# Kernel optimization log

Measured on AMD Instinct MI355X. Metric: run time of the kernel, lower is better.

## Reference

```python
import jax, jax.numpy as jnp
import numpy as np

HEADS = 8
DIM_HEAD = 64
RADIUS = 0.2
NSAMPLE = 8
EPS = 1e-5


def setup_inputs() -> dict:
    key = jax.random.key(0)
    ks = jax.random.split(key, 6)
    b, l, n, dim = 2, 4, 1024, 512
    inner = HEADS * DIM_HEAD
    xyzs = jax.random.uniform(ks[0], (b, l, n, 3), jnp.float32)
    feature = jax.random.normal(ks[1], (b, l, n, dim), jnp.float32)
    gamma = jnp.ones((dim,), jnp.float32)
    beta = jnp.zeros((dim,), jnp.float32)
    w_qkv = jax.random.normal(ks[2], (dim, 3 * inner), jnp.float32) * 0.02
    w_spatial = jax.random.normal(ks[3], (3, DIM_HEAD), jnp.float32) * 0.02
    w_out = jax.random.normal(ks[4], (inner, dim), jnp.float32) * 0.02
    b_out = jnp.zeros((dim,), jnp.float32)
    return {"xyzs": xyzs, "feature": feature, "gamma": gamma, "beta": beta,
            "w_qkv": w_qkv, "w_spatial": w_spatial, "w_out": w_out, "b_out": b_out}


def ball_query(ref, query):
    """pointnet2-style ball query. ref:(B,N,3), query:(B,M,3) -> (B,M,NSAMPLE) int32.
    Takes the first (lowest-index) NSAMPLE in-radius points, pads with the first
    found index; all-zeros if no point is in radius (matches CUDA kernel)."""
    d2 = jnp.sum((query[:, :, None, :] - ref[:, None, :, :]) ** 2, axis=-1)  # (B,M,N)
    mask = d2 < RADIUS ** 2
    nref = ref.shape[1]
    score = jnp.where(mask, -jnp.arange(nref, dtype=jnp.float32), -jnp.inf)
    vals, pos = jax.lax.top_k(score, NSAMPLE)  # smallest in-radius indices first
    valid = vals > -jnp.inf
    first = jnp.where(valid[..., :1], pos[..., :1], 0)
    return jnp.where(valid, pos, first)


def _forward(xyzs, feature, gamma, beta, w_qkv, w_spatial, w_out, b_out):
    b, l, n, dim = feature.shape
    h, dh = HEADS, DIM_HEAD
    inner = h * dh
    scale = dh ** -0.5
    # LayerNorm over channel dim
    mu = jnp.mean(feature, -1, keepdims=True)
    var = jnp.var(feature, -1, keepdims=True)
    normf = (feature - mu) * jax.lax.rsqrt(var + EPS) * gamma + beta
    qkv = normf @ w_qkv
    q, k, v = jnp.split(qkv, 3, axis=-1)          # each (b, l, n, inner)
    xyz_flat = xyzs.reshape(b * l, n, 3)
    k_flat = k.reshape(b * l, n, inner)
    v_flat = v.reshape(b * l, n, inner)
    bidx = jnp.arange(b * l)[:, None, None]

    def per_frame(q_i, xyz_i):
        # q_i: (b, n, inner) queries of frame i; xyz_i: (b, n, 3)
        # frame-i points query neighbors inside every frame of the video
        qxyz = jnp.broadcast_to(xyz_i[:, None], (b, l, n, 3)).reshape(b * l, n, 3)
        idx = ball_query(xyz_flat, qxyz)           # (b*l, n, 8)
        g_k = k_flat[bidx, idx]                    # (b*l, n, 8, inner)
        g_v = v_flat[bidx, idx]
        g_xyz = xyz_flat[bidx, idx]                # (b*l, n, 8, 3)
        disp = g_xyz - qxyz[:, :, None]            # (b*l, n, 8, 3)
        # '(b l) n k (h d) -> b n h (l k) d'
        keys = g_k.reshape(b, l, n, NSAMPLE, h, dh).transpose(0, 2, 4, 1, 3, 5).reshape(b, n, h, l * NSAMPLE, dh)
        vals = g_v.reshape(b, l, n, NSAMPLE, h, dh).transpose(0, 2, 4, 1, 3, 5).reshape(b, n, h, l * NSAMPLE, dh)
        qh = q_i.reshape(b, n, h, dh)
        logits = jnp.einsum('bnhd,bnhjd->bnhj', qh, keys) * scale
        attn = jax.nn.softmax(logits, axis=-1)     # (b, n, h, l*8)
        # 'b l n k d -> b n (l k) d'
        dis = disp.reshape(b, l, n, NSAMPLE, 3).transpose(0, 2, 1, 3, 4).reshape(b, n, l * NSAMPLE, 3)
        dis_attn = jnp.max(attn[..., None] * dis[:, :, None], axis=3)  # (b, n, h, 3)
        dis_attn = (dis_attn @ w_spatial).reshape(b, n, inner)         # spatial_op
        attnout = jnp.einsum('bnhj,bnhjd->bnhd', attn, vals).reshape(b, n, inner)
        return attnout + dis_attn

    q_frames = jnp.moveaxis(q, 1, 0)               # (l, b, n, inner)
    xyz_frames = jnp.moveaxis(xyzs, 1, 0)          # (l, b, n, 3)
    frames = jax.vmap(per_frame)(q_frames, xyz_frames)   # (l, b, n, inner)
    frame_result = jnp.moveaxis(frames, 0, 1)      # (b, l, n, inner)
    out = jax.nn.gelu(frame_result @ w_out + b_out, approximate=False)
    return out + feature


def reference(xyzs, feature, gamma, beta, w_qkv, w_spatial, w_out, b_out):
    return _forward(xyzs, feature, gamma, beta, w_qkv, w_spatial, w_out, b_out)
```

## Files before the change

### kernel.cpp

```cpp
#include <hip/hip_runtime.h>
#include <hip/hip_bf16.h>

#define B_ 2
#define L_ 4
#define N_ 1024
#define DIM_ 512
#define INNER_ 512
#define HEADS_ 8
#define DH_ 64
#define NS_ 8
#define NFR_ (B_ * L_)
#define ROWS_ (B_ * L_ * N_)

typedef unsigned short u16;
typedef __attribute__((ext_vector_type(8))) short bf16x8;
typedef __attribute__((ext_vector_type(4))) float f32x4;

__device__ inline float bf2f(u16 u) {
    union { unsigned i; float f; } c; c.i = ((unsigned)u) << 16; return c.f;
}
__device__ inline float bflo(unsigned v) {
    union { unsigned i; float f; } c; c.i = v << 16; return c.f;
}
__device__ inline float bfhi(unsigned v) {
    union { unsigned i; float f; } c; c.i = v & 0xffff0000u; return c.f;
}
__device__ inline u16 f2bf(float x) {
    __hip_bfloat16 h = __float2bfloat16(x);
    return *reinterpret_cast<u16*>(&h);
}

#if __has_builtin(__builtin_amdgcn_fdot2_f32_bf16)
typedef __bf16 bf2v __attribute__((ext_vector_type(2)));
__device__ inline float dot8(bf16x8 a, bf16x8 b, float acc) {
    union U { bf16x8 v; bf2v p[4]; };
    U ua, ub; ua.v = a; ub.v = b;
    #pragma unroll
    for (int i = 0; i < 4; ++i)
        acc = __builtin_amdgcn_fdot2_f32_bf16(ua.p[i], ub.p[i], acc, false);
    return acc;
}
#else
__device__ inline float dot8(bf16x8 a, bf16x8 b, float acc) {
    #pragma unroll
    for (int e = 0; e < 8; ++e) acc += bf2f((u16)a[e]) * bf2f((u16)b[e]);
    return acc;
}
#endif

__global__ __launch_bounds__(256) void transpose_cvt(
    const float* __restrict__ wqkv, const float* __restrict__ wout,
    u16* __restrict__ wqkvT, u16* __restrict__ woutT)
{
    const float* src; u16* dst; int R, C, tr, tc;
    int b = blockIdx.x;
    if (b < 192) { src = wqkv; dst = wqkvT; R = 512; C = 1536; tr = b / 24; tc = b % 24; }
    else { b -= 192; src = wout; dst = woutT; R = 512; C = 512; tr = b / 8; tc = b % 8; }
    int r0 = tr * 64, c0 = tc * 64;
    int t = threadIdx.x;

    __shared__ float tile[64][65];

    int rr = t >> 2, cs = (t & 3) * 16;
    const float* sp = src + (size_t)(r0 + rr) * C + c0 + cs;
    #pragma unroll
    for (int e = 0; e < 16; e += 4) {
        f32x4 v = *(const f32x4*)(sp + e);
        tile[rr][cs + e + 0] = v[0];
        tile[rr][cs + e + 1] = v[1];
        tile[rr][cs + e + 2] = v[2];
        tile[rr][cs + e + 3] = v[3];
    }
    __syncthreads();

    int c = t >> 2, ks = (t & 3) * 16;
    u16 outv[16];
    #pragma unroll
    for (int e = 0; e < 16; ++e) outv[e] = f2bf(tile[ks + e][c]);
    u16* dp = dst + (size_t)(c0 + c) * R + r0 + ks;
    *(bf16x8*)(dp)     = *(bf16x8*)&outv[0];
    *(bf16x8*)(dp + 8) = *(bf16x8*)&outv[8];
}

__global__ __launch_bounds__(256) void ln_kernel(
    const float* __restrict__ f, const float* __restrict__ g,
    const float* __restrict__ b, u16* __restrict__ o)
{
    int row = blockIdx.x;
    int t = threadIdx.x;
    const float* fr = f + (size_t)row * DIM_;
    float x0 = fr[t], x1 = fr[t + 256];

    __shared__ float red[4];
    float s = x0 + x1;
    #pragma unroll
    for (int off = 32; off; off >>= 1) s += __shfl_xor(s, off, 64);
    if ((t & 63) == 0) red[t >> 6] = s;
    __syncthreads();
    float mu = (red[0] + red[1] + red[2] + red[3]) * (1.0f / 512.0f);
    __syncthreads();

    float d0 = x0 - mu, d1 = x1 - mu;
    float q = d0 * d0 + d1 * d1;
    #pragma unroll
    for (int off = 32; off; off >>= 1) q += __shfl_xor(q, off, 64);
    if ((t & 63) == 0) red[t >> 6] = q;
    __syncthreads();
    float var = (red[0] + red[1] + red[2] + red[3]) * (1.0f / 512.0f);
    float inv = rsqrtf(var + 1e-5f);

    o[(size_t)row * DIM_ + t]       = f2bf(d0 * inv * g[t]       + b[t]);
    o[(size_t)row * DIM_ + t + 256] = f2bf(d1 * inv * g[t + 256] + b[t + 256]);
}

__global__ __launch_bounds__(256) void gemm_bt(
    const u16* __restrict__ A, const u16* __restrict__ Bt,
    u16* __restrict__ Cb16, float* __restrict__ Cf32,
    int M, int N, int K, int nb128, int mode,
    const float* __restrict__ bias, const float* __restrict__ resid)
{
    __shared__ u16 As[128 * 40];
    __shared__ u16 Bs[128 * 40];

    int bx = blockIdx.x % nb128;
    int by = blockIdx.x / nb128;
    int m0 = by * 128, n0 = bx * 128;
    int t = threadIdx.x;
    int wave = t >> 6, lane = t & 63;
    int lr = lane & 15, quad = lane >> 4;
    int wm = (wave >> 1) * 64, wn = (wave & 1) * 64;

    f32x4 acc[4][4];
    #pragma unroll
    for (int i = 0; i < 4; ++i)
        #pragma unroll
        for (int j = 0; j < 4; ++j)
            acc[i][j] = {0.f, 0.f, 0.f, 0.f};

    for (int k0 = 0; k0 < K; k0 += 32) {
        #pragma unroll
        for (int p = 0; p < 2; ++p) {
            int c = t + p * 256;
            int r = c >> 2;
            int kc = (c & 3) * 8;
            *(bf16x8*)&As[r * 40 + kc] = *(const bf16x8*)(A + (size_t)(m0 + r) * K + k0 + kc);
            *(bf16x8*)&Bs[r * 40 + kc] = *(const bf16x8*)(Bt + (size_t)(n0 + r) * K + k0 + kc);
        }
        __syncthreads();

        bf16x8 af[4], bfr[4];
        #pragma unroll
        for (int mb = 0; mb < 4; ++mb)
            af[mb] = *(const bf16x8*)&As[(wm + mb * 16 + lr) * 40 + quad * 8];
        #pragma unroll
        for (int nb = 0; nb < 4; ++nb)
            bfr[nb] = *(const bf16x8*)&Bs[(wn + nb * 16 + lr) * 40 + quad * 8];
        #pragma unroll
        for (int mb = 0; mb < 4; ++mb)
            #pragma unroll
            for (int nb = 0; nb < 4; ++nb)
                acc[mb][nb] = __builtin_amdgcn_mfma_f32_16x16x32_bf16(
                    af[mb], bfr[nb], acc[mb][nb], 0, 0, 0);
        __syncthreads();
    }

    #pragma unroll
    for (int mb = 0; mb < 4; ++mb) {
        #pragma unroll
        for (int nb = 0; nb < 4; ++nb) {
            int col = n0 + wn + nb * 16 + lr;
            #pragma unroll
            for (int r = 0; r < 4; ++r) {
                int row = m0 + wm + mb * 16 + quad * 4 + r;
                float x = acc[mb][nb][r];
                if (mode == 1) {
                    x += bias[col];
                    float gl = 0.5f * x * (1.0f + erff(x * 0.70710678118654752f));
                    Cf32[(size_t)row * N + col] = gl + resid[(size_t)row * N + col];
                } else {
                    Cb16[(size_t)row * N + col] = f2bf(x);
                }
            }
        }
    }
}

#define RPAD_(r) ((r) + ((r) >> 4))

__global__ __launch_bounds__(256) void ballq_kernel(
    const float* __restrict__ xyz, int* __restrict__ idxt)
{
    #pragma clang fp contract(off)
    int chunk = blockIdx.x & 255;
    int combo = blockIdx.x >> 8;
    int jf = combo & 3;
    int bi = combo >> 2;

    __shared__ float rx[N_ + (N_ >> 4)], ry[N_ + (N_ >> 4)], rz[N_ + (N_ >> 4)];
    const float* ref = xyz + (size_t)((bi * L_ + jf) * N_) * 3;
    for (int p = threadIdx.x; p < N_; p += 256) {
        rx[RPAD_(p)] = ref[p * 3 + 0];
        ry[RPAD_(p)] = ref[p * 3 + 1];
        rz[RPAD_(p)] = ref[p * 3 + 2];
    }
    __syncthreads();

    int wave = threadIdx.x >> 6;
    int lane = threadIdx.x & 63;
    int n = chunk * 4 + wave;
    int base = lane * 17;
    int r0 = lane * 16;

    for (int qi = 0; qi < L_; ++qi) {
        const float* qp = xyz + (size_t)((bi * L_ + qi) * N_ + n) * 3;
        float qx = qp[0], qy = qp[1], qz = qp[2];

        unsigned mask = 0;
        #pragma unroll
        for (int j = 0; j < 16; ++j) {
            float dx = qx - rx[base + j];
            float dy = qy - ry[base + j];
            float dz = qz - rz[base + j];
            float d2 = dx * dx + dy * dy;
            d2 = d2 + dz * dz;
            if (d2 < 0.04f) mask |= (1u << j);
        }

        int cnt = __popc(mask);
        int x = cnt;
        #pragma unroll
        for (int off = 1; off < 64; off <<= 1) {
            int y = __shfl_up(x, off, 64);
            if (lane >= off) x += y;
        }
        int pre = x - cnt;
        int total = __shfl(x, 63, 64);

        int localFirst = mask ? (r0 + __builtin_ctz(mask)) : 0x7fffffff;
        int gfirst = localFirst;
        #pragma unroll
        for (int off = 32; off; off >>= 1) gfirst = min(gfirst, __shfl_xor(gfirst, off, 64));

        int* o = idxt + ((size_t)((qi * B_ + bi) * N_ + n)) * 32 + jf * NS_;

        unsigned m = mask;
        int pos = pre;
        while (m && pos < NS_) {
            int j = __builtin_ctz(m);
            o[pos] = r0 + j;
            m &= m - 1;
            ++pos;
        }
        if (lane == 0) {
            int padv = (total > 0) ? gfirst : 0;
            for (int s = (total < NS_ ? total : NS_); s < NS_; ++s) o[s] = padv;
        }
    }
}

__global__ __launch_bounds__(256, 4) void attn_kernel(
    const float* __restrict__ xyz, const u16* __restrict__ qkv,
    const int* __restrict__ idxt, const float* __restrict__ wsp,
    u16* __restrict__ fres)
{
    int x = blockIdx.x & 7;
    int bi = x >> 2;
    int qi = x & 3;
    int n = blockIdx.x >> 3;

    int wave = threadIdx.x >> 6;
    int lane = threadIdx.x & 63;
    int hh = lane >> 5;
    int j = lane & 31;
    int h = wave * 2 + hh;
    int jf = j >> 3;

    int qrow = (bi * L_ + qi) * N_ + n;
    int qq = (qi * B_ + bi) * N_ + n;

    __shared__ float a_s[HEADS_][32];
    __shared__ int grow_s[32];
    __shared__ float da_s[HEADS_][3];

    int idx = idxt[(size_t)qq * 32 + j];
    int kr = (bi * L_ + jf) * N_ + idx;

    const u16* qp = qkv + (size_t)qrow * 1536 + h * 64;
    const u16* kp = qkv + (size_t)kr * 1536 + 512 + h * 64;
    bf16x8 qv[8], kv[8];
    #pragma unroll
    for (int c = 0; c < 8; ++c) {
        kv[c] = *(const bf16x8*)(kp + c * 8);
        qv[c] = *(const bf16x8*)(qp + c * 8);
    }
    float nx = xyz[(size_t)kr * 3 + 0];
    float ny = xyz[(size_t)kr * 3 + 1];
    float nz = xyz[(size_t)kr * 3 + 2];
    __builtin_amdgcn_sched_barrier(0);

    float acc = 0.f;
    #pragma unroll
    for (int c = 0; c < 8; ++c) acc = dot8(kv[c], qv[c], acc);
    float lg = acc * 0.125f;

    float mx = lg;
    #pragma unroll
    for (int off = 16; off; off >>= 1) mx = fmaxf(mx, __shfl_xor(mx, off, 64));
    float e = expf(lg - mx);
    float sum = e;
    #pragma unroll
    for (int off = 16; off; off >>= 1) sum += __shfl_xor(sum, off, 64);
    float a = e / sum;
    a_s[h][j] = a;
    if (wave == 0 && hh == 0) grow_s[j] = kr;

    float qx = xyz[(size_t)qrow * 3 + 0];
    float qy = xyz[(size_t)qrow * 3 + 1];
    float qz = xyz[(size_t)qrow * 3 + 2];
    float tx = a * (nx - qx);
    float ty = a * (ny - qy);
    float tz = a * (nz - qz);
    #pragma unroll
    for (int off = 16; off; off >>= 1) {
        tx = fmaxf(tx, __shfl_xor(tx, off, 64));
        ty = fmaxf(ty, __shfl_xor(ty, off, 64));
        tz = fmaxf(tz, __shfl_xor(tz, off, 64));
    }
    if (j == 0) { da_s[h][0] = tx; da_s[h][1] = ty; da_s[h][2] = tz; }

    __syncthreads();

    int dd = (lane & 31) * 2;
    const u16* vbase = qkv + 1024 + h * 64 + dd;
    int rows[32];
    #pragma unroll
    for (int t = 0; t < 32; ++t) rows[t] = grow_s[t];
    unsigned vv[32];
    #pragma unroll
    for (int t = 0; t < 32; ++t)
        vv[t] = *(const unsigned*)(vbase + (size_t)rows[t] * 1536);
    __builtin_amdgcn_sched_barrier(0);

    float o0 = 0.f, o1 = 0.f;
    #pragma unroll
    for (int t = 0; t < 32; ++t) {
        float at = a_s[h][t];
        o0 += at * bflo(vv[t]);
        o1 += at * bfhi(vv[t]);
    }
    float dax = da_s[h][0], day = da_s[h][1], daz = da_s[h][2];
    float sp0 = dax * wsp[dd]     + day * wsp[64 + dd]     + daz * wsp[128 + dd];
    float sp1 = dax * wsp[dd + 1] + day * wsp[64 + dd + 1] + daz * wsp[128 + dd + 1];

    u16* op = fres + (size_t)qrow * INNER_ + h * 64 + dd;
    unsigned outw = (unsigned)f2bf(o0 + sp0) | ((unsigned)f2bf(o1 + sp1) << 16);
    *(unsigned*)op = outw;
}

extern "C" void kernel_launch(void* const* d_in, const int* in_sizes, int n_in,
                              void* d_out, int out_size, void* d_ws, size_t ws_size,
                              hipStream_t stream) {
    const float* xyz   = (const float*)d_in[0];
    const float* feat  = (const float*)d_in[1];
    const float* gamma = (const float*)d_in[2];
    const float* beta  = (const float*)d_in[3];
    const float* wqkv  = (const float*)d_in[4];
    const float* wsp   = (const float*)d_in[5];
    const float* wout  = (const float*)d_in[6];
    const float* bout  = (const float*)d_in[7];
    float* out = (float*)d_out;

    char* ws = (char*)d_ws;
    u16* normf = (u16*)ws;                 ws += (size_t)ROWS_ * DIM_ * 2;
    u16* wqkvT = (u16*)ws;                 ws += (size_t)3 * INNER_ * DIM_ * 2;
    u16* woutT = (u16*)ws;                 ws += (size_t)DIM_ * INNER_ * 2;
    u16* qkv   = (u16*)ws;                 ws += (size_t)ROWS_ * 3 * INNER_ * 2;
    int* idxt  = (int*)ws;                 ws += (size_t)L_ * NFR_ * N_ * NS_ * 4;
    u16* fres  = normf;

    transpose_cvt<<<256, 256, 0, stream>>>(wqkv, wout, wqkvT, woutT);
    ln_kernel<<<ROWS_, 256, 0, stream>>>(feat, gamma, beta, normf);
    gemm_bt<<<64 * 12, 256, 0, stream>>>(normf, wqkvT, qkv, nullptr,
                                         ROWS_, 3 * INNER_, DIM_, 12, 0, nullptr, nullptr);
    ballq_kernel<<<8 * 256, 256, 0, stream>>>(xyz, idxt);
    attn_kernel<<<ROWS_, 256, 0, stream>>>(xyz, qkv, idxt, wsp, fres);
    gemm_bt<<<64 * 4, 256, 0, stream>>>(fres, woutT, nullptr, out,
                                        ROWS_, DIM_, INNER_, 4, 1, bout, feat);
}
```

Measured before the change: 220.9 us.

## Restructure attention kernel to one wave per head with 512 threads

The attention kernel now runs 512 threads per query, one wave per head. QK dot products are split into 8 pieces of 8 channels each, reduced with lane shuffles. The value accumulation gives each lane one output channel instead of two, and neighbor row indices are staged once in shared memory. The aim is more parallelism and fewer registers per thread, at the cost of an extra barrier, narrower 16-bit value loads and more shuffle reductions.

```diff
diff --git a/kernel.cpp b/kernel.cpp
--- a/kernel.cpp
+++ b/kernel.cpp
@@ -18,12 +18,6 @@
 
 __device__ inline float bf2f(u16 u) {
     union { unsigned i; float f; } c; c.i = ((unsigned)u) << 16; return c.f;
-}
-__device__ inline float bflo(unsigned v) {
-    union { unsigned i; float f; } c; c.i = v << 16; return c.f;
-}
-__device__ inline float bfhi(unsigned v) {
-    union { unsigned i; float f; } c; c.i = v & 0xffff0000u; return c.f;
 }
 __device__ inline u16 f2bf(float x) {
     __hip_bfloat16 h = __float2bfloat16(x);
@@ -258,7 +252,7 @@
     }
 }
 
-__global__ __launch_bounds__(256, 4) void attn_kernel(
+__global__ __launch_bounds__(512, 4) void attn_kernel(
     const float* __restrict__ xyz, const u16* __restrict__ qkv,
     const int* __restrict__ idxt, const float* __restrict__ wsp,
     u16* __restrict__ fres)
@@ -268,93 +262,98 @@
     int qi = x & 3;
     int n = blockIdx.x >> 3;
 
-    int wave = threadIdx.x >> 6;
-    int lane = threadIdx.x & 63;
-    int hh = lane >> 5;
-    int j = lane & 31;
-    int h = wave * 2 + hh;
-    int jf = j >> 3;
+    int t = threadIdx.x;
+    int h = t >> 6;
+    int lane = t & 63;
+    int piece = lane >> 3;
+    int jg = lane & 7;
 
     int qrow = (bi * L_ + qi) * N_ + n;
     int qq = (qi * B_ + bi) * N_ + n;
 
+    __shared__ int kr_s[32];
     __shared__ float a_s[HEADS_][32];
-    __shared__ int grow_s[32];
     __shared__ float da_s[HEADS_][3];
 
-    int idx = idxt[(size_t)qq * 32 + j];
-    int kr = (bi * L_ + jf) * N_ + idx;
-
-    const u16* qp = qkv + (size_t)qrow * 1536 + h * 64;
-    const u16* kp = qkv + (size_t)kr * 1536 + 512 + h * 64;
-    bf16x8 qv[8], kv[8];
-    #pragma unroll
-    for (int c = 0; c < 8; ++c) {
-        kv[c] = *(const bf16x8*)(kp + c * 8);
-        qv[c] = *(const bf16x8*)(qp + c * 8);
-    }
-    float nx = xyz[(size_t)kr * 3 + 0];
-    float ny = xyz[(size_t)kr * 3 + 1];
-    float nz = xyz[(size_t)kr * 3 + 2];
+    if (t < 32) {
+        int idx = idxt[(size_t)qq * 32 + t];
+        kr_s[t] = (bi * L_ + (t >> 3)) * N_ + idx;
+    }
+    __syncthreads();
+
+    bf16x8 qv = *(const bf16x8*)(qkv + (size_t)qrow * 1536 + h * 64 + piece * 8);
+
+    float part[4];
+    #pragma unroll
+    for (int g = 0; g < 4; ++g) {
+        int row = kr_s[g * 8 + jg];
+        bf16x8 kv = *(const bf16x8*)(qkv + (size_t)row * 1536 + 512 + h * 64 + piece * 8);
+        part[g] = dot8(kv, qv, 0.f);
+    }
+    #pragma unroll
+    for (int g = 0; g < 4; ++g) {
+        #pragma unroll
+        for (int off = 8; off < 64; off <<= 1)
+            part[g] += __shfl_xor(part[g], off, 64);
+        part[g] *= 0.125f;
+    }
+
+    float mx = fmaxf(fmaxf(part[0], part[1]), fmaxf(part[2], part[3]));
+    #pragma unroll
+    for (int off = 1; off < 8; off <<= 1) mx = fmaxf(mx, __shfl_xor(mx, off, 64));
+    float e[4], sum = 0.f;
+    #pragma unroll
+    for (int g = 0; g < 4; ++g) { e[g] = expf(part[g] - mx); sum += e[g]; }
+    #pragma unroll
+    for (int off = 1; off < 8; off <<= 1) sum += __shfl_xor(sum, off, 64);
+    float inv = 1.0f / sum;
+
+    if (piece == 0) {
+        #pragma unroll
+        for (int g = 0; g < 4; ++g) a_s[h][g * 8 + jg] = e[g] * inv;
+
+        float qx = xyz[(size_t)qrow * 3 + 0];
+        float qy = xyz[(size_t)qrow * 3 + 1];
+        float qz = xyz[(size_t)qrow * 3 + 2];
+        float tx, ty, tz;
+        #pragma unroll
+        for (int g = 0; g < 4; ++g) {
+            int row = kr_s[g * 8 + jg];
+            float a = e[g] * inv;
+            float gx = a * (xyz[(size_t)row * 3 + 0] - qx);
+            float gy = a * (xyz[(size_t)row * 3 + 1] - qy);
+            float gz = a * (xyz[(size_t)row * 3 + 2] - qz);
+            if (g == 0) { tx = gx; ty = gy; tz = gz; }
+            else { tx = fmaxf(tx, gx); ty = fmaxf(ty, gy); tz = fmaxf(tz, gz); }
+        }
+        #pragma unroll
+        for (int off = 1; off < 8; off <<= 1) {
+            tx = fmaxf(tx, __shfl_xor(tx, off, 64));
+            ty = fmaxf(ty, __shfl_xor(ty, off, 64));
+            tz = fmaxf(tz, __shfl_xor(tz, off, 64));
+        }
+        if (jg == 0) { da_s[h][0] = tx; da_s[h][1] = ty; da_s[h][2] = tz; }
+    }
+
+    __syncthreads();
+
+    int d = lane;
+    const u16* vbase = qkv + 1024 + h * 64 + d;
+    int rows[32];
+    #pragma unroll
+    for (int tt = 0; tt < 32; ++tt) rows[tt] = kr_s[tt];
+    u16 vv[32];
+    #pragma unroll
+    for (int tt = 0; tt < 32; ++tt)
+        vv[tt] = *(vbase + (size_t)rows[tt] * 1536);
     __builtin_amdgcn_sched_barrier(0);
 
-    float acc = 0.f;
-    #pragma unroll
-    for (int c = 0; c < 8; ++c) acc = dot8(kv[c], qv[c], acc);
-    float lg = acc * 0.125f;
-
-    float mx = lg;
-    #pragma unroll
-    for (int off = 16; off; off >>= 1) mx = fmaxf(mx, __shfl_xor(mx, off, 64));
-    float e = expf(lg - mx);
-    float sum = e;
-    #pragma unroll
-    for (int off = 16; off; off >>= 1) sum += __shfl_xor(sum, off, 64);
-    float a = e / sum;
-    a_s[h][j] = a;
-    if (wave == 0 && hh == 0) grow_s[j] = kr;
-
-    float qx = xyz[(size_t)qrow * 3 + 0];
-    float qy = xyz[(size_t)qrow * 3 + 1];
-    float qz = xyz[(size_t)qrow * 3 + 2];
-    float tx = a * (nx - qx);
-    float ty = a * (ny - qy);
-    float tz = a * (nz - qz);
-    #pragma unroll
-    for (int off = 16; off; off >>= 1) {
-        tx = fmaxf(tx, __shfl_xor(tx, off, 64));
-        ty = fmaxf(ty, __shfl_xor(ty, off, 64));
-        tz = fmaxf(tz, __shfl_xor(tz, off, 64));
-    }
-    if (j == 0) { da_s[h][0] = tx; da_s[h][1] = ty; da_s[h][2] = tz; }
-
-    __syncthreads();
-
-    int dd = (lane & 31) * 2;
-    const u16* vbase = qkv + 1024 + h * 64 + dd;
-    int rows[32];
-    #pragma unroll
-    for (int t = 0; t < 32; ++t) rows[t] = grow_s[t];
-    unsigned vv[32];
-    #pragma unroll
-    for (int t = 0; t < 32; ++t)
-        vv[t] = *(const unsigned*)(vbase + (size_t)rows[t] * 1536);
-    __builtin_amdgcn_sched_barrier(0);
-
-    float o0 = 0.f, o1 = 0.f;
-    #pragma unroll
-    for (int t = 0; t < 32; ++t) {
-        float at = a_s[h][t];
-        o0 += at * bflo(vv[t]);
-        o1 += at * bfhi(vv[t]);
-    }
-    float dax = da_s[h][0], day = da_s[h][1], daz = da_s[h][2];
-    float sp0 = dax * wsp[dd]     + day * wsp[64 + dd]     + daz * wsp[128 + dd];
-    float sp1 = dax * wsp[dd + 1] + day * wsp[64 + dd + 1] + daz * wsp[128 + dd + 1];
-
-    u16* op = fres + (size_t)qrow * INNER_ + h * 64 + dd;
-    unsigned outw = (unsigned)f2bf(o0 + sp0) | ((unsigned)f2bf(o1 + sp1) << 16);
-    *(unsigned*)op = outw;
+    float o = 0.f;
+    #pragma unroll
+    for (int tt = 0; tt < 32; ++tt) o += a_s[h][tt] * bf2f(vv[tt]);
+
+    float sp = da_s[h][0] * wsp[d] + da_s[h][1] * wsp[64 + d] + da_s[h][2] * wsp[128 + d];
+    fres[(size_t)qrow * INNER_ + h * 64 + d] = f2bf(o + sp);
 }
 
 extern "C" void kernel_launch(void* const* d_in, const int* in_sizes, int n_in,
@@ -383,7 +382,7 @@
     gemm_bt<<<64 * 12, 256, 0, stream>>>(normf, wqkvT, qkv, nullptr,
                                          ROWS_, 3 * INNER_, DIM_, 12, 0, nullptr, nullptr);
     ballq_kernel<<<8 * 256, 256, 0, stream>>>(xyz, idxt);
-    attn_kernel<<<ROWS_, 256, 0, stream>>>(xyz, qkv, idxt, wsp, fres);
+    attn_kernel<<<ROWS_, 512, 0, stream>>>(xyz, qkv, idxt, wsp, fres);
     gemm_bt<<<64 * 4, 256, 0, stream>>>(fres, woutT, nullptr, out,
                                         ROWS_, DIM_, INNER_, 4, 1, bout, feat);
 }
```

After: 233.2 us. 5.6% more time.
